# Performance work log

Measured on AMD Instinct MI355X. Metric: run time of the kernel, lower is better.

Reference implementation:

```python
import jax, jax.numpy as jnp
import numpy as np

BATCH = 16
C = 4          # num classes; also used for self.c in the original (undefined there, fixed here)
H = W = 512
LAMBD = 0.005
SMOOTH = 1e-6


def setup_inputs() -> dict:
    key = jax.random.key(0)
    k1, k2 = jax.random.split(key)
    inp = jax.random.normal(k1, (BATCH, C, H, W), dtype=jnp.float32)
    tgt = jax.random.normal(k2, (BATCH, C, H, W), dtype=jnp.float32)
    return {"input": inp, "target": tgt}


def reference(input, target):
    B = BATCH
    N = 2 * B
    # evidential confidence weighting
    mm_evidence = jax.nn.softplus(target)
    mm_alpha = mm_evidence + 1.0
    mm_S = jnp.sum(mm_alpha, axis=1, keepdims=True)          # [B,1,H,W]
    confidence = jnp.exp(-(jnp.float32(C) / mm_S))
    inp = jax.nn.softmax(input + 1.0, axis=1)
    tgt = jax.nn.softmax((target + 1.0) * confidence, axis=1)
    z1 = jnp.concatenate([inp, tgt], axis=0)                 # [N,C,H,W]
    z2 = jnp.concatenate([tgt, inp], axis=0)
    # pairwise dice: algebraic form of the NxNxCxHxW broadcast reduction
    zf1 = z1.reshape(N, -1)                                  # [N, C*H*W]
    zf2 = z2.reshape(N, -1)
    intersect = zf1 @ zf2.T                                  # [N,N]
    z_sum = jnp.sum(zf1 * zf1, axis=1)[:, None]              # row sums of squares
    y_sum = jnp.sum(zf2 * zf2, axis=1)[None, :]              # col sums of squares
    D = (2.0 * intersect + SMOOTH) / (z_sum + y_sum + SMOOTH)
    # mask out the (i, B+i) / (B+i, i) positive pairs
    idx = jnp.arange(N)
    mask = ~((idx[:, None] == idx[None, :] - B) | (idx[:, None] == idx[None, :] + B))
    D = D * mask.astype(D.dtype)
    diag = jnp.diagonal(D)
    on_diag = jnp.sum((diag - 1.0) ** 2)
    off_diag = jnp.sum(D ** 2) - jnp.sum(diag ** 2)
    return on_diag + LAMBD * off_diag
```

## Files before the change

### kernel.cpp

```cpp
#include <hip/hip_runtime.h>
#include <math.h>

#define HWSZ 262144
#define NCOPY 16
#define LAMBD 0.005f
#define SMOOTH 1e-6f

typedef __attribute__((ext_vector_type(8))) short bf16x8;
typedef __attribute__((ext_vector_type(4))) float f32x4;
typedef __attribute__((ext_vector_type(4))) int i32x4;

static __device__ __forceinline__ float rcp_hw(float x) {
    float r; asm("v_rcp_f32 %0, %1" : "=v"(r) : "v"(x)); return r;
}
static __device__ __forceinline__ unsigned int pk_bf16(float lo, float hi) {
    unsigned int r;
    asm("v_cvt_pk_bf16_f32 %0, %1, %2" : "=v"(r) : "v"(lo), "v"(hi));
    return r;
}

__global__ __launch_bounds__(256) void gram_kernel(
    const float* __restrict__ X,
    const float* __restrict__ T,
    float* __restrict__ Gpart)
{
    __shared__ unsigned short w[32][264];

    const int tid  = threadIdx.x;
    const int b    = tid >> 4;
    const int px4  = (tid & 15) << 2;
    const int lane = tid & 63;
    const int wv   = tid >> 6;
    const int r    = lane & 15;
    const int g    = lane >> 4;
    const int I    = (wv >> 1) << 4;
    const int J    = (wv & 1) << 4;

    const int pixBase = blockIdx.x << 6;

    float fi[16], ft[16];
    #pragma unroll
    for (int c = 0; c < 4; ++c) {
        size_t off = (size_t)(b * 4 + c) * HWSZ + pixBase + px4;
        *(float4*)&fi[c * 4] = *(const float4*)(X + off);
        *(float4*)&ft[c * 4] = *(const float4*)(T + off);
    }

    unsigned int pu[8], qu[8];
    #pragma unroll
    for (int p = 0; p < 4; ++p) {
        float t0 = ft[p], t1 = ft[4 + p], t2 = ft[8 + p], t3 = ft[12 + p];

        float prod = (1.f + __expf(t0)) * (1.f + __expf(t1))
                   * (1.f + __expf(t2)) * (1.f + __expf(t3));
        float S    = __logf(prod) + 4.0f;
        float conf = __expf(-4.0f * rcp_hw(S));

        float e0 = __expf(fi[p]),     e1 = __expf(fi[4 + p]);
        float e2 = __expf(fi[8 + p]), e3 = __expf(fi[12 + p]);
        float inv = rcp_hw(e0 + e1 + e2 + e3);
        pu[p * 2]     = pk_bf16(e0 * inv, e1 * inv);
        pu[p * 2 + 1] = pk_bf16(e2 * inv, e3 * inv);

        float q0 = __expf(fmaf(t0, conf, conf));
        float q1 = __expf(fmaf(t1, conf, conf));
        float q2 = __expf(fmaf(t2, conf, conf));
        float q3 = __expf(fmaf(t3, conf, conf));
        float qi = rcp_hw(q0 + q1 + q2 + q3);
        qu[p * 2]     = pk_bf16(q0 * qi, q1 * qi);
        qu[p * 2 + 1] = pk_bf16(q2 * qi, q3 * qi);
    }

    *(i32x4*)&w[b][px4 * 4]          = *(const i32x4*)&pu[0];
    *(i32x4*)&w[b][px4 * 4 + 8]      = *(const i32x4*)&pu[4];
    *(i32x4*)&w[16 + b][px4 * 4]     = *(const i32x4*)&qu[0];
    *(i32x4*)&w[16 + b][px4 * 4 + 8] = *(const i32x4*)&qu[4];
    __syncthreads();

    f32x4 acc = {0.f, 0.f, 0.f, 0.f};
    #pragma unroll
    for (int kc = 0; kc < 8; ++kc) {
        bf16x8 a  = *(const bf16x8*)&w[I + r][kc * 32 + g * 8];
        bf16x8 bb = *(const bf16x8*)&w[J + r][kc * 32 + g * 8];
        acc = __builtin_amdgcn_mfma_f32_16x16x32_bf16(a, bb, acc, 0, 0, 0);
    }

    float* dst = Gpart + (size_t)(blockIdx.x & (NCOPY - 1)) * 1024;
    #pragma unroll
    for (int v = 0; v < 4; ++v) {
        int row = I + g * 4 + v;
        int col = J + r;
        atomicAdd(&dst[row * 32 + col], acc[v]);
    }
}

__global__ __launch_bounds__(256) void loss_kernel(
    const float* __restrict__ Gpart, float* __restrict__ out)
{
    __shared__ float G[1024];
    __shared__ float red[4];
    const int t = threadIdx.x;

    for (int e = t; e < 1024; e += 256) {
        float s = 0.f;
        #pragma unroll
        for (int c = 0; c < NCOPY; ++c) s += Gpart[c * 1024 + e];
        G[e] = s;
    }
    __syncthreads();

    float local = 0.f;
    for (int e = t; e < 1024; e += 256) {
        int i = e >> 5, j = e & 31;
        float num = 2.f * G[(i << 5) | (j ^ 16)] + SMOOTH;
        float den = G[i * 33] + G[(j ^ 16) * 33] + SMOOTH;
        float D = num / den;
        if (j == (i ^ 16)) D = 0.f;
        local += (i == j) ? (D - 1.f) * (D - 1.f) : LAMBD * D * D;
    }

    #pragma unroll
    for (int off = 32; off; off >>= 1) local += __shfl_down(local, off);
    if ((t & 63) == 0) red[t >> 6] = local;
    __syncthreads();
    if (t == 0) out[0] = red[0] + red[1] + red[2] + red[3];
}

extern "C" void kernel_launch(void* const* d_in, const int* in_sizes, int n_in,
                              void* d_out, int out_size, void* d_ws, size_t ws_size,
                              hipStream_t stream)
{
    const float* X = (const float*)d_in[0];
    const float* T = (const float*)d_in[1];
    float* Gpart = (float*)d_ws;

    hipMemsetAsync(Gpart, 0, NCOPY * 1024 * sizeof(float), stream);
    gram_kernel<<<4096, 256, 0, stream>>>(X, T, Gpart);
    loss_kernel<<<1, 256, 0, stream>>>(Gpart, (float*)d_out);
}
```

Measured before the change: 40.60 us.

## Process four pixel tiles per block with register-prefetched double buffering

Each gram block now covers four 64-pixel tiles instead of one, so the grid shrinks from 4096 to 1024 blocks. The next tile's inputs are prefetched into registers while the current tile is computed, and LDS is double-buffered. MFMA accumulation stays in registers across tiles, which cuts the global atomic adds by a factor of four. The loss kernel's partial-sum reduction is also vectorized to float4. In exchange there is more register pressure and fewer blocks to hide latency with.

New measurement: 36.17 us. -10.9%, faster.

```diff
diff --git a/kernel.cpp b/kernel.cpp
--- a/kernel.cpp
+++ b/kernel.cpp
@@ -24,7 +24,7 @@
     const float* __restrict__ T,
     float* __restrict__ Gpart)
 {
-    __shared__ unsigned short w[32][264];
+    __shared__ unsigned short w[2][32][264];
 
     const int tid  = threadIdx.x;
     const int b    = tid >> 4;
@@ -36,53 +36,70 @@
     const int I    = (wv >> 1) << 4;
     const int J    = (wv & 1) << 4;
 
-    const int pixBase = blockIdx.x << 6;
+    const int tile0 = blockIdx.x << 2;
 
-    float fi[16], ft[16];
+    float fr[2][16], tr[2][16];
+
     #pragma unroll
     for (int c = 0; c < 4; ++c) {
-        size_t off = (size_t)(b * 4 + c) * HWSZ + pixBase + px4;
-        *(float4*)&fi[c * 4] = *(const float4*)(X + off);
-        *(float4*)&ft[c * 4] = *(const float4*)(T + off);
+        size_t off = (size_t)(b * 4 + c) * HWSZ + (tile0 << 6) + px4;
+        *(float4*)&fr[0][c * 4] = *(const float4*)(X + off);
+        *(float4*)&tr[0][c * 4] = *(const float4*)(T + off);
     }
 
-    unsigned int pu[8], qu[8];
-    #pragma unroll
-    for (int p = 0; p < 4; ++p) {
-        float t0 = ft[p], t1 = ft[4 + p], t2 = ft[8 + p], t3 = ft[12 + p];
+    f32x4 acc = {0.f, 0.f, 0.f, 0.f};
 
-        float prod = (1.f + __expf(t0)) * (1.f + __expf(t1))
-                   * (1.f + __expf(t2)) * (1.f + __expf(t3));
-        float S    = __logf(prod) + 4.0f;
-        float conf = __expf(-4.0f * rcp_hw(S));
+    #pragma unroll 4
+    for (int t = 0; t < 4; ++t) {
+        const int cur = t & 1, nxt = cur ^ 1;
 
-        float e0 = __expf(fi[p]),     e1 = __expf(fi[4 + p]);
-        float e2 = __expf(fi[8 + p]), e3 = __expf(fi[12 + p]);
-        float inv = rcp_hw(e0 + e1 + e2 + e3);
-        pu[p * 2]     = pk_bf16(e0 * inv, e1 * inv);
-        pu[p * 2 + 1] = pk_bf16(e2 * inv, e3 * inv);
+        if (t < 3) {
+            #pragma unroll
+            for (int c = 0; c < 4; ++c) {
+                size_t off = (size_t)(b * 4 + c) * HWSZ + ((tile0 + t + 1) << 6) + px4;
+                *(float4*)&fr[nxt][c * 4] = *(const float4*)(X + off);
+                *(float4*)&tr[nxt][c * 4] = *(const float4*)(T + off);
+            }
+        }
 
-        float q0 = __expf(fmaf(t0, conf, conf));
-        float q1 = __expf(fmaf(t1, conf, conf));
-        float q2 = __expf(fmaf(t2, conf, conf));
-        float q3 = __expf(fmaf(t3, conf, conf));
-        float qi = rcp_hw(q0 + q1 + q2 + q3);
-        qu[p * 2]     = pk_bf16(q0 * qi, q1 * qi);
-        qu[p * 2 + 1] = pk_bf16(q2 * qi, q3 * qi);
-    }
+        unsigned int pu[8], qu[8];
+        #pragma unroll
+        for (int p = 0; p < 4; ++p) {
+            float t0 = tr[cur][p],     t1 = tr[cur][4 + p];
+            float t2 = tr[cur][8 + p], t3 = tr[cur][12 + p];
 
-    *(i32x4*)&w[b][px4 * 4]          = *(const i32x4*)&pu[0];
-    *(i32x4*)&w[b][px4 * 4 + 8]      = *(const i32x4*)&pu[4];
-    *(i32x4*)&w[16 + b][px4 * 4]     = *(const i32x4*)&qu[0];
-    *(i32x4*)&w[16 + b][px4 * 4 + 8] = *(const i32x4*)&qu[4];
-    __syncthreads();
+            float prod = (1.f + __expf(t0)) * (1.f + __expf(t1))
+                       * (1.f + __expf(t2)) * (1.f + __expf(t3));
+            float S    = __logf(prod) + 4.0f;
+            float conf = __expf(-4.0f * rcp_hw(S));
 
-    f32x4 acc = {0.f, 0.f, 0.f, 0.f};
-    #pragma unroll
-    for (int kc = 0; kc < 8; ++kc) {
-        bf16x8 a  = *(const bf16x8*)&w[I + r][kc * 32 + g * 8];
-        bf16x8 bb = *(const bf16x8*)&w[J + r][kc * 32 + g * 8];
-        acc = __builtin_amdgcn_mfma_f32_16x16x32_bf16(a, bb, acc, 0, 0, 0);
+            float e0 = __expf(fr[cur][p]),     e1 = __expf(fr[cur][4 + p]);
+            float e2 = __expf(fr[cur][8 + p]), e3 = __expf(fr[cur][12 + p]);
+            float inv = rcp_hw(e0 + e1 + e2 + e3);
+            pu[p * 2]     = pk_bf16(e0 * inv, e1 * inv);
+            pu[p * 2 + 1] = pk_bf16(e2 * inv, e3 * inv);
+
+            float q0 = __expf(fmaf(t0, conf, conf));
+            float q1 = __expf(fmaf(t1, conf, conf));
+            float q2 = __expf(fmaf(t2, conf, conf));
+            float q3 = __expf(fmaf(t3, conf, conf));
+            float qi = rcp_hw(q0 + q1 + q2 + q3);
+            qu[p * 2]     = pk_bf16(q0 * qi, q1 * qi);
+            qu[p * 2 + 1] = pk_bf16(q2 * qi, q3 * qi);
+        }
+
+        *(i32x4*)&w[cur][b][px4 * 4]          = *(const i32x4*)&pu[0];
+        *(i32x4*)&w[cur][b][px4 * 4 + 8]      = *(const i32x4*)&pu[4];
+        *(i32x4*)&w[cur][16 + b][px4 * 4]     = *(const i32x4*)&qu[0];
+        *(i32x4*)&w[cur][16 + b][px4 * 4 + 8] = *(const i32x4*)&qu[4];
+        __syncthreads();
+
+        #pragma unroll
+        for (int kc = 0; kc < 8; ++kc) {
+            bf16x8 a  = *(const bf16x8*)&w[cur][I + r][kc * 32 + g * 8];
+            bf16x8 bb = *(const bf16x8*)&w[cur][J + r][kc * 32 + g * 8];
+            acc = __builtin_amdgcn_mfma_f32_16x16x32_bf16(a, bb, acc, 0, 0, 0);
+        }
     }
 
     float* dst = Gpart + (size_t)(blockIdx.x & (NCOPY - 1)) * 1024;
@@ -101,11 +118,12 @@
     __shared__ float red[4];
     const int t = threadIdx.x;
 
-    for (int e = t; e < 1024; e += 256) {
-        float s = 0.f;
+    {
+        f32x4 s = {0.f, 0.f, 0.f, 0.f};
         #pragma unroll
-        for (int c = 0; c < NCOPY; ++c) s += Gpart[c * 1024 + e];
-        G[e] = s;
+        for (int c = 0; c < NCOPY; ++c)
+            s += *(const f32x4*)&Gpart[c * 1024 + t * 4];
+        *(f32x4*)&G[t * 4] = s;
     }
     __syncthreads();
 
@@ -135,6 +153,6 @@
     float* Gpart = (float*)d_ws;
 
     hipMemsetAsync(Gpart, 0, NCOPY * 1024 * sizeof(float), stream);
-    gram_kernel<<<4096, 256, 0, stream>>>(X, T, Gpart);
+    gram_kernel<<<1024, 256, 0, stream>>>(X, T, Gpart);
     loss_kernel<<<1, 256, 0, stream>>>(Gpart, (float*)d_out);
 }
```

## Build MFMA operands in registers, compute three Gram blocks, and loop per wave

Applied to the files above, without the earlier changes.

Each wave now loads its pixels directly in MFMA operand layout and feeds the computed softmax values to MFMA from registers, with no LDS staging. It accumulates only the PP, PQ and QQ 16x16 blocks, using the symmetry of the 32x32 Gram matrix. Each wave runs four iterations with double-buffered prefetch, so the grid shrinks by four and there are fewer atomics. Block results are combined through LDS before a single set of atomics per block, and the loss kernel is adapted to the three-block form.

After: 42.29 us. 4.2% more time.

```diff
diff --git a/kernel.cpp b/kernel.cpp
--- a/kernel.cpp
+++ b/kernel.cpp
@@ -5,10 +5,10 @@
 #define NCOPY 16
 #define LAMBD 0.005f
 #define SMOOTH 1e-6f
+#define ITERS 4
 
 typedef __attribute__((ext_vector_type(8))) short bf16x8;
 typedef __attribute__((ext_vector_type(4))) float f32x4;
-typedef __attribute__((ext_vector_type(4))) int i32x4;
 
 static __device__ __forceinline__ float rcp_hw(float x) {
     float r; asm("v_rcp_f32 %0, %1" : "=v"(r) : "v"(x)); return r;
@@ -24,99 +24,119 @@
     const float* __restrict__ T,
     float* __restrict__ Gpart)
 {
-    __shared__ unsigned short w[32][264];
-
     const int tid  = threadIdx.x;
-    const int b    = tid >> 4;
-    const int px4  = (tid & 15) << 2;
     const int lane = tid & 63;
     const int wv   = tid >> 6;
     const int r    = lane & 15;
     const int g    = lane >> 4;
-    const int I    = (wv >> 1) << 4;
-    const int J    = (wv & 1) << 4;
 
-    const int pixBase = blockIdx.x << 6;
+    const int waveId = blockIdx.x * 4 + wv;
+    const size_t base = (size_t)waveId * 64 + g * 4;
 
-    float fi[16], ft[16];
+    const float* Xb = X + (size_t)r * 4 * HWSZ + base;
+    const float* Tb = T + (size_t)r * 4 * HWSZ + base;
+
+    f32x4 accPP = {0,0,0,0}, accPQ = {0,0,0,0}, accQQ = {0,0,0,0};
+
+    f32x4 fin[2][4], ttn[2][4];
     #pragma unroll
     for (int c = 0; c < 4; ++c) {
-        size_t off = (size_t)(b * 4 + c) * HWSZ + pixBase + px4;
-        *(float4*)&fi[c * 4] = *(const float4*)(X + off);
-        *(float4*)&ft[c * 4] = *(const float4*)(T + off);
+        fin[0][c] = *(const f32x4*)(Xb + c * HWSZ);
+        ttn[0][c] = *(const f32x4*)(Tb + c * HWSZ);
     }
 
-    unsigned int pu[8], qu[8];
     #pragma unroll
-    for (int p = 0; p < 4; ++p) {
-        float t0 = ft[p], t1 = ft[4 + p], t2 = ft[8 + p], t3 = ft[12 + p];
+    for (int it = 0; it < ITERS; ++it) {
+        const int cur = it & 1, nxt = cur ^ 1;
+        if (it + 1 < ITERS) {
+            #pragma unroll
+            for (int c = 0; c < 4; ++c) {
+                fin[nxt][c] = *(const f32x4*)(Xb + c * HWSZ + (it + 1) * 16);
+                ttn[nxt][c] = *(const f32x4*)(Tb + c * HWSZ + (it + 1) * 16);
+            }
+        }
 
-        float prod = (1.f + __expf(t0)) * (1.f + __expf(t1))
-                   * (1.f + __expf(t2)) * (1.f + __expf(t3));
-        float S    = __logf(prod) + 4.0f;
-        float conf = __expf(-4.0f * rcp_hw(S));
+        unsigned int pf[8], qf[8];
+        #pragma unroll
+        for (int u = 0; u < 4; ++u) {
+            float t0 = ttn[cur][0][u], t1 = ttn[cur][1][u],
+                  t2 = ttn[cur][2][u], t3 = ttn[cur][3][u];
 
-        float e0 = __expf(fi[p]),     e1 = __expf(fi[4 + p]);
-        float e2 = __expf(fi[8 + p]), e3 = __expf(fi[12 + p]);
-        float inv = rcp_hw(e0 + e1 + e2 + e3);
-        pu[p * 2]     = pk_bf16(e0 * inv, e1 * inv);
-        pu[p * 2 + 1] = pk_bf16(e2 * inv, e3 * inv);
+            float prod = (1.f + __expf(t0)) * (1.f + __expf(t1))
+                       * (1.f + __expf(t2)) * (1.f + __expf(t3));
+            float S    = __logf(prod) + 4.0f;
+            float conf = __expf(-4.0f * rcp_hw(S));
 
-        float q0 = __expf(fmaf(t0, conf, conf));
-        float q1 = __expf(fmaf(t1, conf, conf));
-        float q2 = __expf(fmaf(t2, conf, conf));
-        float q3 = __expf(fmaf(t3, conf, conf));
-        float qi = rcp_hw(q0 + q1 + q2 + q3);
-        qu[p * 2]     = pk_bf16(q0 * qi, q1 * qi);
-        qu[p * 2 + 1] = pk_bf16(q2 * qi, q3 * qi);
+            float e0 = __expf(fin[cur][0][u]), e1 = __expf(fin[cur][1][u]);
+            float e2 = __expf(fin[cur][2][u]), e3 = __expf(fin[cur][3][u]);
+            float inv = rcp_hw(e0 + e1 + e2 + e3);
+            pf[u * 2]     = pk_bf16(e0 * inv, e1 * inv);
+            pf[u * 2 + 1] = pk_bf16(e2 * inv, e3 * inv);
+
+            float q0 = __expf(fmaf(t0, conf, conf));
+            float q1 = __expf(fmaf(t1, conf, conf));
+            float q2 = __expf(fmaf(t2, conf, conf));
+            float q3 = __expf(fmaf(t3, conf, conf));
+            float qi = rcp_hw(q0 + q1 + q2 + q3);
+            qf[u * 2]     = pk_bf16(q0 * qi, q1 * qi);
+            qf[u * 2 + 1] = pk_bf16(q2 * qi, q3 * qi);
+        }
+
+        bf16x8 Pa = *(const bf16x8*)&pf[0], Pb = *(const bf16x8*)&pf[4];
+        bf16x8 Qa = *(const bf16x8*)&qf[0], Qb = *(const bf16x8*)&qf[4];
+        accPP = __builtin_amdgcn_mfma_f32_16x16x32_bf16(Pa, Pa, accPP, 0, 0, 0);
+        accPQ = __builtin_amdgcn_mfma_f32_16x16x32_bf16(Pa, Qa, accPQ, 0, 0, 0);
+        accQQ = __builtin_amdgcn_mfma_f32_16x16x32_bf16(Qa, Qa, accQQ, 0, 0, 0);
+        accPP = __builtin_amdgcn_mfma_f32_16x16x32_bf16(Pb, Pb, accPP, 0, 0, 0);
+        accPQ = __builtin_amdgcn_mfma_f32_16x16x32_bf16(Pb, Qb, accPQ, 0, 0, 0);
+        accQQ = __builtin_amdgcn_mfma_f32_16x16x32_bf16(Qb, Qb, accQQ, 0, 0, 0);
     }
 
-    *(i32x4*)&w[b][px4 * 4]          = *(const i32x4*)&pu[0];
-    *(i32x4*)&w[b][px4 * 4 + 8]      = *(const i32x4*)&pu[4];
-    *(i32x4*)&w[16 + b][px4 * 4]     = *(const i32x4*)&qu[0];
-    *(i32x4*)&w[16 + b][px4 * 4 + 8] = *(const i32x4*)&qu[4];
+    __shared__ float Gs[4][768];
+    #pragma unroll
+    for (int v = 0; v < 4; ++v) {
+        int idx = (g * 4 + v) * 16 + r;
+        Gs[wv][idx]       = accPP[v];
+        Gs[wv][256 + idx] = accPQ[v];
+        Gs[wv][512 + idx] = accQQ[v];
+    }
     __syncthreads();
 
-    f32x4 acc = {0.f, 0.f, 0.f, 0.f};
-    #pragma unroll
-    for (int kc = 0; kc < 8; ++kc) {
-        bf16x8 a  = *(const bf16x8*)&w[I + r][kc * 32 + g * 8];
-        bf16x8 bb = *(const bf16x8*)&w[J + r][kc * 32 + g * 8];
-        acc = __builtin_amdgcn_mfma_f32_16x16x32_bf16(a, bb, acc, 0, 0, 0);
-    }
-
-    float* dst = Gpart + (size_t)(blockIdx.x & (NCOPY - 1)) * 1024;
-    #pragma unroll
-    for (int v = 0; v < 4; ++v) {
-        int row = I + g * 4 + v;
-        int col = J + r;
-        atomicAdd(&dst[row * 32 + col], acc[v]);
-    }
+    float* dst = Gpart + (size_t)(blockIdx.x & (NCOPY - 1)) * 768;
+    for (int e = tid; e < 768; e += 256)
+        atomicAdd(&dst[e], Gs[0][e] + Gs[1][e] + Gs[2][e] + Gs[3][e]);
 }
 
 __global__ __launch_bounds__(256) void loss_kernel(
     const float* __restrict__ Gpart, float* __restrict__ out)
 {
-    __shared__ float G[1024];
+    __shared__ float G[768];
     __shared__ float red[4];
     const int t = threadIdx.x;
 
-    for (int e = t; e < 1024; e += 256) {
+    for (int e = t; e < 768; e += 256) {
         float s = 0.f;
         #pragma unroll
-        for (int c = 0; c < NCOPY; ++c) s += Gpart[c * 1024 + e];
+        for (int c = 0; c < NCOPY; ++c) s += Gpart[c * 768 + e];
         G[e] = s;
     }
     __syncthreads();
 
+    const float* PP = G;
+    const float* QQ = G + 512;
+    const int i = t >> 4, j = t & 15;
     float local = 0.f;
-    for (int e = t; e < 1024; e += 256) {
-        int i = e >> 5, j = e & 31;
-        float num = 2.f * G[(i << 5) | (j ^ 16)] + SMOOTH;
-        float den = G[i * 33] + G[(j ^ 16) * 33] + SMOOTH;
-        float D = num / den;
-        if (j == (i ^ 16)) D = 0.f;
-        local += (i == j) ? (D - 1.f) * (D - 1.f) : LAMBD * D * D;
+    {
+        float D = (2.f * G[t] + SMOOTH) / (PP[i * 17] + PP[j * 17] + SMOOTH);
+        if (i != j) local += LAMBD * D * D;
+    }
+    {
+        float D = (2.f * G[256 + t] + SMOOTH) / (PP[i * 17] + QQ[j * 17] + SMOOTH);
+        local += (i == j) ? 2.f * (D - 1.f) * (D - 1.f) : 2.f * LAMBD * D * D;
+    }
+    {
+        float D = (2.f * G[512 + t] + SMOOTH) / (QQ[i * 17] + QQ[j * 17] + SMOOTH);
+        if (i != j) local += LAMBD * D * D;
     }
 
     #pragma unroll
@@ -134,7 +154,7 @@
     const float* T = (const float*)d_in[1];
     float* Gpart = (float*)d_ws;
 
-    hipMemsetAsync(Gpart, 0, NCOPY * 1024 * sizeof(float), stream);
-    gram_kernel<<<4096, 256, 0, stream>>>(X, T, Gpart);
+    hipMemsetAsync(Gpart, 0, NCOPY * 768 * sizeof(float), stream);
+    gram_kernel<<<1024, 256, 0, stream>>>(X, T, Gpart);
     loss_kernel<<<1, 256, 0, stream>>>(Gpart, (float*)d_out);
 }
```
